# Kernel tuning notes

Hardware: AMD Instinct MI355X
Metric: run time of the kernel (lower is better)

The kernel has to match this reference:

```python
import jax, jax.numpy as jnp
import numpy as np

ENC_H, DEC_H, ATTN = 1024, 1024, 512
B, S = 32, 4096


def setup_inputs() -> dict:
    key = jax.random.key(0)
    k1, k2, k3, k4, k5, k6 = jax.random.split(key, 6)
    decoder_state = jax.random.normal(k1, (B, DEC_H), dtype=jnp.float32)
    encoder_outputs = jax.random.normal(k2, (B, S, ENC_H), dtype=jnp.float32)
    mask = jax.random.randint(k3, (B, S), 0, 2, dtype=jnp.int32)
    W_h = jax.random.normal(k4, (ENC_H, ATTN), dtype=jnp.float32) / np.sqrt(ENC_H)
    W_s = jax.random.normal(k5, (DEC_H, ATTN), dtype=jnp.float32) / np.sqrt(DEC_H)
    v = jax.random.normal(k6, (ATTN,), dtype=jnp.float32) / np.sqrt(ATTN)
    return {"decoder_state": decoder_state, "encoder_outputs": encoder_outputs,
            "mask": mask, "W_h": W_h, "W_s": W_s, "v": v}


def reference(decoder_state, encoder_outputs, mask, W_h, W_s, v):
    # proj_enc: (B, S, A), proj_dec: (B, 1, A)
    proj_enc = jnp.einsum('bse,ea->bsa', encoder_outputs, W_h)
    proj_dec = jnp.einsum('bd,da->ba', decoder_state, W_s)[:, None, :]
    # scores: (B, S) = v^T tanh(W_h h_j + W_s s_i)
    scores = jnp.einsum('bsa,a->bs', jnp.tanh(proj_enc + proj_dec), v)
    neg_inf = jnp.finfo(scores.dtype).min
    scores = jnp.where(mask == 0, neg_inf, scores)
    weights = jax.nn.softmax(scores, axis=-1)  # (B, S)
    context = jnp.einsum('bs,bse->be', weights, encoder_outputs)  # (B, ENC_H)
    return context, weights
```

## Files before the change

kernel.cpp:

```cpp
#include <hip/hip_runtime.h>
#include <hip/hip_bf16.h>
#include <float.h>
#include <math.h>

#define NB 32
#define NS 4096
#define NE 1024
#define ND 1024
#define NA 512

typedef __attribute__((ext_vector_type(4))) float f32x4;
typedef __attribute__((ext_vector_type(8))) short short8;
typedef __attribute__((ext_vector_type(4))) short short4v;
typedef __attribute__((address_space(3))) char lds_char_t;
typedef __attribute__((address_space(1))) const char g_char_t;

static __device__ __forceinline__ ushort f2bf(float f){
    union { float f; unsigned int u; } x; x.f = f;
    unsigned int u = x.u + 0x7fffu + ((x.u >> 16) & 1u);
    return (ushort)(u >> 16);
}

__global__ __launch_bounds__(256) void k_prep_wht(const float* __restrict__ Wh,
                                                  ushort* __restrict__ WT){
    int i = blockIdx.x * 256 + threadIdx.x;
    int k = i >> 9, a = i & 511;
    WT[a * 1024 + k] = f2bf(Wh[i]);
}

__global__ __launch_bounds__(512) void k_projdec(const float* __restrict__ dec,
                                                 const float* __restrict__ Ws,
                                                 float* __restrict__ pdp){
    int b = blockIdx.x >> 2, kc = blockIdx.x & 3;
    int a = threadIdx.x;
    const float* dp = dec + b * ND + kc * 256;
    const float* wp = Ws + (size_t)(kc * 256) * NA + a;
    float acc = 0.f;
    #pragma unroll 4
    for (int k = 0; k < 256; k++) acc += dp[k] * wp[(size_t)k * NA];
    pdp[(kc * NB + b) * NA + a] = acc;
}

__global__ __launch_bounds__(512, 4) void k_scores(const float* __restrict__ E,
                                                   const ushort* __restrict__ WT,
                                                   const float* __restrict__ pdp,
                                                   const float* __restrict__ v,
                                                   float* __restrict__ scores){
    const int t = threadIdx.x;
    const int wave = t >> 6, lane = t & 63;
    const int grp = lane >> 4, l15 = lane & 15;
    const int b = blockIdx.x >> 6;
    const int s0 = (blockIdx.x & 63) << 6;

    __shared__ __align__(16) float  f32t[2][64 * 64];
    __shared__ __align__(16) ushort bft[64 * 64];
    __shared__ float sc[64][8];

    const int c0 = wave * 128 + lane;
    const int c1 = c0 + 64;
    const float* g0 = E + ((size_t)(b * NS + s0 + (c0 >> 4))) * NE + (c0 & 15) * 4;
    const float* g1 = E + ((size_t)(b * NS + s0 + (c1 >> 4))) * NE + (c1 & 15) * 4;

    f32x4 acc[4][4];
    f32x4 zero; zero[0]=0.f; zero[1]=0.f; zero[2]=0.f; zero[3]=0.f;
    #pragma unroll
    for (int m = 0; m < 4; m++)
        #pragma unroll
        for (int n = 0; n < 4; n++) acc[m][n] = zero;

    auto dma = [&](int buf, int it){
        char* l0 = (char*)&f32t[buf][0] + c0 * 16;
        char* l1 = (char*)&f32t[buf][0] + c1 * 16;
        __builtin_amdgcn_global_load_lds((g_char_t*)(g0 + it * 64), (lds_char_t*)l0, 16, 0, 0);
        __builtin_amdgcn_global_load_lds((g_char_t*)(g1 + it * 64), (lds_char_t*)l1, 16, 0, 0);
    };

    auto convert = [&](int buf){
        const f32x4* src = (const f32x4*)&f32t[buf][0];
        f32x4 alo = src[t];
        f32x4 ahi = src[t + 512];
        int rlo = t >> 4, rhi = 32 + rlo;
        unsigned colb = (unsigned)((t & 15) * 8);
        short4v hlo, hhi;
        #pragma unroll
        for (int e = 0; e < 4; e++){ hlo[e] = (short)f2bf(alo[e]); hhi[e] = (short)f2bf(ahi[e]); }
        unsigned blo = ((unsigned)(rlo * 128) + colb) ^ ((unsigned)(rlo & 7) << 4);
        unsigned bhi = ((unsigned)(rhi * 128) + colb) ^ ((unsigned)(rhi & 7) << 4);
        *(short4v*)((char*)bft + blo) = hlo;
        *(short4v*)((char*)bft + bhi) = hhi;
    };

    auto compute = [&](int it){
        #pragma unroll
        for (int kk = 0; kk < 2; kk++){
            short8 af[4], bfr[4];
            #pragma unroll
            for (int m = 0; m < 4; m++){
                int row = m * 16 + l15;
                unsigned off = (unsigned)(row * 128 + kk * 64 + grp * 16);
                af[m] = *(const short8*)((const char*)bft + (off ^ ((unsigned)(row & 7) << 4)));
            }
            #pragma unroll
            for (int n = 0; n < 4; n++){
                int c = wave * 64 + n * 16 + l15;
                bfr[n] = *(const short8*)(WT + (size_t)c * 1024 + it * 64 + kk * 32 + grp * 8);
            }
            #pragma unroll
            for (int m = 0; m < 4; m++)
                #pragma unroll
                for (int n = 0; n < 4; n++)
                    acc[m][n] = __builtin_amdgcn_mfma_f32_16x16x32_bf16(af[m], bfr[n], acc[m][n], 0, 0, 0);
        }
    };

    dma(0, 0);
    asm volatile("s_waitcnt vmcnt(0)" ::: "memory");
    __builtin_amdgcn_s_barrier();
    asm volatile("" ::: "memory");

    for (int it = 0; it < 16; it++){
        if (it < 15) dma((it + 1) & 1, it + 1);
        convert(it & 1);
        asm volatile("s_waitcnt lgkmcnt(0)" ::: "memory");
        __builtin_amdgcn_s_barrier();
        asm volatile("" ::: "memory");
        compute(it);
        asm volatile("s_waitcnt vmcnt(0) lgkmcnt(0)" ::: "memory");
        __builtin_amdgcn_s_barrier();
        asm volatile("" ::: "memory");
    }

    float pdc[4], vc[4];
    #pragma unroll
    for (int n = 0; n < 4; n++){
        int c = wave * 64 + n * 16 + l15;
        float p = 0.f;
        #pragma unroll
        for (int kc = 0; kc < 4; kc++) p += pdp[(kc * NB + b) * NA + c];
        pdc[n] = p;
        vc[n] = v[c];
    }
    #pragma unroll
    for (int m = 0; m < 4; m++){
        #pragma unroll
        for (int j = 0; j < 4; j++){
            float s = 0.f;
            #pragma unroll
            for (int n = 0; n < 4; n++) s += tanhf(acc[m][n][j] + pdc[n]) * vc[n];
            s += __shfl_xor(s, 1);
            s += __shfl_xor(s, 2);
            s += __shfl_xor(s, 4);
            s += __shfl_xor(s, 8);
            if (l15 == 0) sc[m * 16 + grp * 4 + j][wave] = s;
        }
    }
    __syncthreads();
    if (t < 64){
        float s = 0.f;
        #pragma unroll
        for (int w = 0; w < 8; w++) s += sc[t][w];
        scores[b * NS + s0 + t] = s;
    }
}

__global__ __launch_bounds__(256) void k_softmax(const float* __restrict__ scores,
                                                 const int* __restrict__ mask,
                                                 float* __restrict__ weights){
    int b = blockIdx.x, t = threadIdx.x;
    __shared__ float red[8];
    float vals[16];
    float mx = -FLT_MAX;
    #pragma unroll
    for (int i = 0; i < 16; i++){
        int s = i * 256 + t;
        float x = scores[b * NS + s];
        x = (mask[b * NS + s] != 0) ? x : -FLT_MAX;
        vals[i] = x;
        mx = fmaxf(mx, x);
    }
    #pragma unroll
    for (int off = 32; off; off >>= 1) mx = fmaxf(mx, __shfl_xor(mx, off));
    int wv = t >> 6;
    if ((t & 63) == 0) red[wv] = mx;
    __syncthreads();
    mx = fmaxf(fmaxf(red[0], red[1]), fmaxf(red[2], red[3]));
    float sum = 0.f;
    #pragma unroll
    for (int i = 0; i < 16; i++){ vals[i] = __expf(vals[i] - mx); sum += vals[i]; }
    #pragma unroll
    for (int off = 32; off; off >>= 1) sum += __shfl_xor(sum, off);
    if ((t & 63) == 0) red[4 + wv] = sum;
    __syncthreads();
    sum = red[4] + red[5] + red[6] + red[7];
    float inv = 1.f / sum;
    #pragma unroll
    for (int i = 0; i < 16; i++) weights[b * NS + i * 256 + t] = vals[i] * inv;
}

__global__ __launch_bounds__(256) void k_context(const float* __restrict__ E,
                                                 const float* __restrict__ weights,
                                                 float* __restrict__ part){
    int b = blockIdx.x >> 3, ch = blockIdx.x & 7;
    int t = threadIdx.x;
    __shared__ float wsm[512];
    wsm[t] = weights[b * NS + ch * 512 + t];
    wsm[256 + t] = weights[b * NS + ch * 512 + 256 + t];
    __syncthreads();
    const f32x4* Ep = (const f32x4*)(E + ((size_t)b * NS + ch * 512) * NE) + t;
    f32x4 acc; acc[0]=0.f; acc[1]=0.f; acc[2]=0.f; acc[3]=0.f;
    #pragma unroll 4
    for (int s = 0; s < 512; s++){
        f32x4 e = Ep[(size_t)s * 256];
        float w = wsm[s];
        acc[0] += w * e[0]; acc[1] += w * e[1];
        acc[2] += w * e[2]; acc[3] += w * e[3];
    }
    float* pp = part + ((size_t)(b * 8 + ch)) * NE + t * 4;
    pp[0] = acc[0]; pp[1] = acc[1]; pp[2] = acc[2]; pp[3] = acc[3];
}

__global__ __launch_bounds__(256) void k_reduce_ctx(const float* __restrict__ part,
                                                    float* __restrict__ ctx){
    int i = blockIdx.x * 256 + threadIdx.x;
    int b = i >> 10, e = i & 1023;
    float s = 0.f;
    #pragma unroll
    for (int ch = 0; ch < 8; ch++) s += part[((size_t)(b * 8 + ch)) * NE + e];
    ctx[i] = s;
}

extern "C" void kernel_launch(void* const* d_in, const int* in_sizes, int n_in,
                              void* d_out, int out_size, void* d_ws, size_t ws_size,
                              hipStream_t stream){
    const float* dec  = (const float*)d_in[0];
    const float* E    = (const float*)d_in[1];
    const int*   mask = (const int*)d_in[2];
    const float* Wh   = (const float*)d_in[3];
    const float* Ws   = (const float*)d_in[4];
    const float* v    = (const float*)d_in[5];
    float* ctx = (float*)d_out;
    float* weights = (float*)d_out + NB * NE;

    char* ws = (char*)d_ws;
    ushort* WT   = (ushort*)ws;
    float*  pdp  = (float*)(ws + (1 << 20));
    float*  scr  = (float*)(ws + (1 << 20) + (256 << 10));
    float*  part = (float*)(ws + (1 << 20) + (256 << 10) + (512 << 10));

    k_prep_wht<<<2048, 256, 0, stream>>>(Wh, WT);
    k_projdec<<<128, 512, 0, stream>>>(dec, Ws, pdp);
    k_scores<<<2048, 512, 0, stream>>>(E, WT, pdp, v, scr);
    k_softmax<<<32, 256, 0, stream>>>(scr, mask, weights);
    k_context<<<256, 256, 0, stream>>>(E, weights, part);
    k_reduce_ctx<<<128, 256, 0, stream>>>(part, ctx);
}
```

Measured before the change: 449.2 us.

## Convert swizzled fp32 LDS tiles to bf16 in registers and widen context blocks

The score kernel drops the separate bf16 staging buffer and its conversion pass. Each wave now reads XOR-swizzled fp32 rows straight from the DMA'd LDS buffer and converts them to bf16 fragments in registers, with one barrier per iteration instead of two. W^T fragments are loaded before the next DMA is issued. The context kernel goes from 256 to 1024 threads per block, splitting the sequence chunk four ways and reducing the partials through LDS, to raise memory-level parallelism. The partial-sum buffer now reuses the W^T workspace region, which is safe only because the score kernel has finished with W^T before the context kernel runs.

```diff
diff --git a/kernel.cpp b/kernel.cpp
--- a/kernel.cpp
+++ b/kernel.cpp
@@ -11,7 +11,6 @@
 
 typedef __attribute__((ext_vector_type(4))) float f32x4;
 typedef __attribute__((ext_vector_type(8))) short short8;
-typedef __attribute__((ext_vector_type(4))) short short4v;
 typedef __attribute__((address_space(3))) char lds_char_t;
 typedef __attribute__((address_space(1))) const char g_char_t;
 
@@ -52,14 +51,16 @@
     const int b = blockIdx.x >> 6;
     const int s0 = (blockIdx.x & 63) << 6;
 
-    __shared__ __align__(16) float  f32t[2][64 * 64];
-    __shared__ __align__(16) ushort bft[64 * 64];
+    __shared__ __align__(16) float f32t[2][64 * 64];
     __shared__ float sc[64][8];
 
     const int c0 = wave * 128 + lane;
     const int c1 = c0 + 64;
-    const float* g0 = E + ((size_t)(b * NS + s0 + (c0 >> 4))) * NE + (c0 & 15) * 4;
-    const float* g1 = E + ((size_t)(b * NS + s0 + (c1 >> 4))) * NE + (c1 & 15) * 4;
+    const int r0 = c0 >> 4, r1 = c1 >> 4;
+    const int sd0 = (c0 & 15) ^ (r0 & 7);
+    const int sd1 = (c1 & 15) ^ (r1 & 7);
+    const float* g0 = E + ((size_t)(b * NS + s0 + r0)) * NE + sd0 * 4;
+    const float* g1 = E + ((size_t)(b * NS + s0 + r1)) * NE + sd1 * 4;
 
     f32x4 acc[4][4];
     f32x4 zero; zero[0]=0.f; zero[1]=0.f; zero[2]=0.f; zero[3]=0.f;
@@ -75,59 +76,45 @@
         __builtin_amdgcn_global_load_lds((g_char_t*)(g1 + it * 64), (lds_char_t*)l1, 16, 0, 0);
     };
 
-    auto convert = [&](int buf){
-        const f32x4* src = (const f32x4*)&f32t[buf][0];
-        f32x4 alo = src[t];
-        f32x4 ahi = src[t + 512];
-        int rlo = t >> 4, rhi = 32 + rlo;
-        unsigned colb = (unsigned)((t & 15) * 8);
-        short4v hlo, hhi;
-        #pragma unroll
-        for (int e = 0; e < 4; e++){ hlo[e] = (short)f2bf(alo[e]); hhi[e] = (short)f2bf(ahi[e]); }
-        unsigned blo = ((unsigned)(rlo * 128) + colb) ^ ((unsigned)(rlo & 7) << 4);
-        unsigned bhi = ((unsigned)(rhi * 128) + colb) ^ ((unsigned)(rhi & 7) << 4);
-        *(short4v*)((char*)bft + blo) = hlo;
-        *(short4v*)((char*)bft + bhi) = hhi;
-    };
-
-    auto compute = [&](int it){
+    dma(0, 0);
+
+    const int cb = wave * 64 + l15;
+
+    for (int it = 0; it < 16; ++it){
+        __syncthreads();
+
+        short8 wt[2][4];
+        const ushort* wbase = WT + it * 64 + grp * 8;
+        #pragma unroll
+        for (int kk = 0; kk < 2; kk++)
+            #pragma unroll
+            for (int n = 0; n < 4; n++)
+                wt[kk][n] = *(const short8*)(wbase + (size_t)(cb + n * 16) * 1024 + kk * 32);
+        __builtin_amdgcn_sched_barrier(0);
+
+        if (it < 15) dma((it + 1) & 1, it + 1);
+        __builtin_amdgcn_sched_barrier(0);
+
+        const char* base = (const char*)&f32t[it & 1][0];
         #pragma unroll
         for (int kk = 0; kk < 2; kk++){
-            short8 af[4], bfr[4];
             #pragma unroll
             for (int m = 0; m < 4; m++){
-                int row = m * 16 + l15;
-                unsigned off = (unsigned)(row * 128 + kk * 64 + grp * 16);
-                af[m] = *(const short8*)((const char*)bft + (off ^ ((unsigned)(row & 7) << 4)));
-            }
-            #pragma unroll
-            for (int n = 0; n < 4; n++){
-                int c = wave * 64 + n * 16 + l15;
-                bfr[n] = *(const short8*)(WT + (size_t)c * 1024 + it * 64 + kk * 32 + grp * 8);
-            }
-            #pragma unroll
-            for (int m = 0; m < 4; m++)
+                const int r = m * 16 + l15;
+                const int scg = kk * 8 + grp * 2;
+                f32x4 lo = *(const f32x4*)(base + r * 256 + ((scg       ^ (r & 7)) << 4));
+                f32x4 hi = *(const f32x4*)(base + r * 256 + (((scg + 1) ^ (r & 7)) << 4));
+                short8 af;
+                #pragma unroll
+                for (int e = 0; e < 4; e++){
+                    af[e]     = (short)__builtin_bit_cast(ushort, __float2bfloat16(lo[e]));
+                    af[e + 4] = (short)__builtin_bit_cast(ushort, __float2bfloat16(hi[e]));
+                }
                 #pragma unroll
                 for (int n = 0; n < 4; n++)
-                    acc[m][n] = __builtin_amdgcn_mfma_f32_16x16x32_bf16(af[m], bfr[n], acc[m][n], 0, 0, 0);
+                    acc[m][n] = __builtin_amdgcn_mfma_f32_16x16x32_bf16(af, wt[kk][n], acc[m][n], 0, 0, 0);
+            }
         }
-    };
-
-    dma(0, 0);
-    asm volatile("s_waitcnt vmcnt(0)" ::: "memory");
-    __builtin_amdgcn_s_barrier();
-    asm volatile("" ::: "memory");
-
-    for (int it = 0; it < 16; it++){
-        if (it < 15) dma((it + 1) & 1, it + 1);
-        convert(it & 1);
-        asm volatile("s_waitcnt lgkmcnt(0)" ::: "memory");
-        __builtin_amdgcn_s_barrier();
-        asm volatile("" ::: "memory");
-        compute(it);
-        asm volatile("s_waitcnt vmcnt(0) lgkmcnt(0)" ::: "memory");
-        __builtin_amdgcn_s_barrier();
-        asm volatile("" ::: "memory");
     }
 
     float pdc[4], vc[4];
@@ -197,26 +184,36 @@
     for (int i = 0; i < 16; i++) weights[b * NS + i * 256 + t] = vals[i] * inv;
 }
 
-__global__ __launch_bounds__(256) void k_context(const float* __restrict__ E,
-                                                 const float* __restrict__ weights,
-                                                 float* __restrict__ part){
+__global__ __launch_bounds__(1024) void k_context(const float* __restrict__ E,
+                                                  const float* __restrict__ weights,
+                                                  float* __restrict__ part){
     int b = blockIdx.x >> 3, ch = blockIdx.x & 7;
     int t = threadIdx.x;
+    int h = t >> 8, tg = t & 255;
     __shared__ float wsm[512];
-    wsm[t] = weights[b * NS + ch * 512 + t];
-    wsm[256 + t] = weights[b * NS + ch * 512 + 256 + t];
-    __syncthreads();
-    const f32x4* Ep = (const f32x4*)(E + ((size_t)b * NS + ch * 512) * NE) + t;
+    __shared__ __align__(16) f32x4 red[4][256];
+    if (t < 512) wsm[t] = weights[b * NS + ch * 512 + t];
+    __syncthreads();
+    const f32x4* Ep = (const f32x4*)(E + ((size_t)b * NS + ch * 512 + h * 128) * NE) + tg;
     f32x4 acc; acc[0]=0.f; acc[1]=0.f; acc[2]=0.f; acc[3]=0.f;
     #pragma unroll 4
-    for (int s = 0; s < 512; s++){
+    for (int s = 0; s < 128; s++){
         f32x4 e = Ep[(size_t)s * 256];
-        float w = wsm[s];
+        float w = wsm[h * 128 + s];
         acc[0] += w * e[0]; acc[1] += w * e[1];
         acc[2] += w * e[2]; acc[3] += w * e[3];
     }
-    float* pp = part + ((size_t)(b * 8 + ch)) * NE + t * 4;
-    pp[0] = acc[0]; pp[1] = acc[1]; pp[2] = acc[2]; pp[3] = acc[3];
+    red[h][tg] = acc;
+    __syncthreads();
+    if (h == 0){
+        f32x4 a0 = red[0][tg], a1 = red[1][tg], a2 = red[2][tg], a3 = red[3][tg];
+        f32x4 s;
+        s[0] = a0[0]+a1[0]+a2[0]+a3[0];
+        s[1] = a0[1]+a1[1]+a2[1]+a3[1];
+        s[2] = a0[2]+a1[2]+a2[2]+a3[2];
+        s[3] = a0[3]+a1[3]+a2[3]+a3[3];
+        *(f32x4*)(part + ((size_t)(b * 8 + ch)) * NE + tg * 4) = s;
+    }
 }
 
 __global__ __launch_bounds__(256) void k_reduce_ctx(const float* __restrict__ part,
@@ -243,14 +240,14 @@
 
     char* ws = (char*)d_ws;
     ushort* WT   = (ushort*)ws;
+    float*  part = (float*)ws;
     float*  pdp  = (float*)(ws + (1 << 20));
     float*  scr  = (float*)(ws + (1 << 20) + (256 << 10));
-    float*  part = (float*)(ws + (1 << 20) + (256 << 10) + (512 << 10));
 
     k_prep_wht<<<2048, 256, 0, stream>>>(Wh, WT);
     k_projdec<<<128, 512, 0, stream>>>(dec, Ws, pdp);
     k_scores<<<2048, 512, 0, stream>>>(E, WT, pdp, v, scr);
     k_softmax<<<32, 256, 0, stream>>>(scr, mask, weights);
-    k_context<<<256, 256, 0, stream>>>(E, weights, part);
+    k_context<<<256, 1024, 0, stream>>>(E, weights, part);
     k_reduce_ctx<<<128, 256, 0, stream>>>(part, ctx);
 }
```

Measured after the change: 432.5 us. 1.04x faster.
